# Performance work log

Hardware: AMD Instinct MI355X
Metric: run time of the kernel (lower is better)

The kernel has to match this reference:

```python
import jax, jax.numpy as jnp
import numpy as np

N_NODES = 100000
N_EDGES = 1600000
F_IN, F_HID, F_OUT = 256, 128, 32


def setup_inputs() -> dict:
    key = jax.random.key(0)
    k1, k2, k3, k4 = jax.random.split(key, 4)
    x = jax.random.normal(k1, (N_NODES, F_IN), dtype=jnp.float32)
    edge_index = jax.random.randint(k2, (2, N_EDGES), 0, N_NODES, dtype=jnp.int64)
    W1 = jax.random.normal(k3, (F_IN, F_HID), dtype=jnp.float32) * (1.0 / np.sqrt(F_IN))
    b1 = jnp.zeros((F_HID,), dtype=jnp.float32)
    W2 = jax.random.normal(k4, (F_HID, F_OUT), dtype=jnp.float32) * (1.0 / np.sqrt(F_HID))
    b2 = jnp.zeros((F_OUT,), dtype=jnp.float32)
    return {"x": x, "edge_index": edge_index, "W1": W1, "b1": b1, "W2": W2, "b2": b2}


def _gcn_norm(edge_index, num_nodes):
    # Add self-loops, then symmetric normalization deg^-1/2[src] * deg^-1/2[dst].
    loops = jnp.arange(num_nodes, dtype=edge_index.dtype)
    src = jnp.concatenate([edge_index[0], loops])
    dst = jnp.concatenate([edge_index[1], loops])
    deg = jax.ops.segment_sum(jnp.ones_like(dst, dtype=jnp.float32), dst,
                              num_segments=num_nodes)
    dinv = jnp.where(deg > 0, jax.lax.rsqrt(deg), 0.0)
    norm = dinv[src] * dinv[dst]  # [E + N]
    return src, dst, norm


def _gcn_conv(h, src, dst, norm, num_nodes):
    # h already linearly transformed. Gather sources, scale, scatter-add to dst.
    msgs = h[src] * norm[:, None]
    return jax.ops.segment_sum(msgs, dst, num_segments=num_nodes)


def reference(x, edge_index, W1, b1, W2, b2):
    n = x.shape[0]
    src, dst, norm = _gcn_norm(edge_index, n)
    # Layer 1: linear -> normalized scatter-add -> bias -> relu
    h = _gcn_conv(x @ W1, src, dst, norm, n) + b1
    h = jax.nn.relu(h)
    # F.dropout with training=False (eval mode) is identity.
    # Layer 2
    out = _gcn_conv(h @ W2, src, dst, norm, n) + b2
    return jax.nn.log_softmax(out, axis=1)
```

## Files before the change

kernel.cpp:

```cpp
#include <hip/hip_runtime.h>

#define N_NODES 100000
#define N_EDGES 1600000
#define F_IN 256
#define F_HID 128
#define F_OUT 32
#define NBUCK 391
#define BIN_BLOCKS 512
#define EDGES_PER_BIN 3125

typedef unsigned short ushort_t;
typedef unsigned int uint_t;

using short8  = __attribute__((ext_vector_type(8))) short;
using floatx4 = __attribute__((ext_vector_type(4))) float;

__device__ __forceinline__ ushort_t f2bf(float f) {
    uint_t u = __float_as_uint(f);
    u += 0x7fff + ((u >> 16) & 1);
    return (ushort_t)(u >> 16);
}
__device__ __forceinline__ float bf_lo(uint_t u) { return __uint_as_float(u << 16); }
__device__ __forceinline__ float bf_hi(uint_t u) { return __uint_as_float(u & 0xffff0000u); }
__device__ __forceinline__ uint_t bfpack_trunc(float a, float b) {
    return __builtin_amdgcn_perm(__float_as_uint(b), __float_as_uint(a), 0x07060302u);
}

__global__ __launch_bounds__(256) void histwt_kernel(const int* __restrict__ ei,
                                                     int* __restrict__ bucket_cnt,
                                                     const float* __restrict__ W1,
                                                     const float* __restrict__ W2,
                                                     ushort_t* __restrict__ W1T,
                                                     ushort_t* __restrict__ W2T) {
    __shared__ int h[NBUCK];
    if (blockIdx.x < BIN_BLOCKS) {
        for (int i = threadIdx.x; i < NBUCK; i += 256) h[i] = 0;
        __syncthreads();
        int gid = blockIdx.x * 256 + threadIdx.x;
        for (int e = gid; e < N_EDGES; e += BIN_BLOCKS * 256)
            atomicAdd(&h[ei[N_EDGES + e] >> 8], 1);
        __syncthreads();
        for (int i = threadIdx.x; i < NBUCK; i += 256) {
            int c = h[i];
            if (c) atomicAdd(&bucket_cnt[i], c);
        }
    } else {
        int t = (blockIdx.x - BIN_BLOCKS) * 256 + threadIdx.x;
#pragma unroll
        for (int j = 0; j < 4; j++) {
            int e = j * 8192 + t;
            int n = e >> 8, k = e & 255;
            W1T[e] = f2bf(W1[k * F_HID + n]);
        }
        if (t < 4096) {
            int n = t >> 7, k = t & 127;
            W2T[t] = f2bf(W2[k * F_OUT + n]);
        }
    }
}

__global__ __launch_bounds__(512) void scan_kernel(const int* __restrict__ bucket_cnt,
                                                   int* __restrict__ bucket_base,
                                                   int* __restrict__ bucket_cursor,
                                                   int* __restrict__ offs) {
    __shared__ int s[512];
    int t = threadIdx.x;
    int own = (t < NBUCK) ? bucket_cnt[t] : 0;
    s[t] = own;
    __syncthreads();
    for (int off = 1; off < 512; off <<= 1) {
        int v = (t >= off) ? s[t - off] : 0;
        __syncthreads();
        s[t] += v;
        __syncthreads();
    }
    if (t < NBUCK) {
        int ex = s[t] - own;
        bucket_base[t] = ex;
        bucket_cursor[t] = ex;
    }
    if (t == 0) {
        bucket_base[NBUCK] = N_EDGES;
        offs[N_NODES] = N_EDGES;
    }
}

__global__ __launch_bounds__(256) void bin_kernel(const int* __restrict__ ei,
                                                  int* __restrict__ bucket_cursor,
                                                  int2* __restrict__ binned) {
    __shared__ int h[NBUCK];
    __shared__ int base[NBUCK];
    const int t = threadIdx.x;
    const int beg = blockIdx.x * EDGES_PER_BIN;
    const int end = beg + EDGES_PER_BIN;
    for (int i = t; i < NBUCK; i += 256) h[i] = 0;
    __syncthreads();
    for (int e = beg + t; e < end; e += 256) atomicAdd(&h[ei[N_EDGES + e] >> 8], 1);
    __syncthreads();
    for (int i = t; i < NBUCK; i += 256) {
        int c = h[i];
        base[i] = c ? atomicAdd(&bucket_cursor[i], c) : 0;
        h[i] = 0;
    }
    __syncthreads();
    for (int e = beg + t; e < end; e += 256) {
        int s = ei[e], d = ei[N_EDGES + e];
        int bk = d >> 8;
        int p = base[bk] + atomicAdd(&h[bk], 1);
        binned[p] = make_int2(s, d);
    }
}

__global__ __launch_bounds__(256) void build_kernel(const int2* __restrict__ binned,
                                                    const int* __restrict__ bucket_base,
                                                    int* __restrict__ offs,
                                                    int* __restrict__ csr,
                                                    float* __restrict__ dinv,
                                                    int* __restrict__ degarr) {
    __shared__ int h[256];
    __shared__ int sc[256];
    __shared__ int cur[256];
    const int b = blockIdx.x, t = threadIdx.x;
    const int beg = bucket_base[b];
    const int end = bucket_base[b + 1];
    h[t] = 0;
    __syncthreads();
    for (int j = beg + t; j < end; j += 256) {
        int2 p = binned[j];
        atomicAdd(&h[p.y & 255], 1);
    }
    __syncthreads();
    int deg = h[t];
    sc[t] = deg;
    __syncthreads();
    for (int off = 1; off < 256; off <<= 1) {
        int v = (t >= off) ? sc[t - off] : 0;
        __syncthreads();
        sc[t] += v;
        __syncthreads();
    }
    int excl = sc[t] - deg;
    cur[t] = excl;
    int node = b * 256 + t;
    if (node < N_NODES) {
        offs[node] = beg + excl;
        dinv[node] = rsqrtf((float)deg + 1.0f);
        degarr[node] = deg;
    }
    __syncthreads();
    for (int j = beg + t; j < end; j += 256) {
        int2 p = binned[j];
        int pos = atomicAdd(&cur[p.y & 255], 1);
        csr[beg + pos] = p.x;
    }
}

__global__ __launch_bounds__(256) void pack_kernel(int* __restrict__ csr,
                                                   const int* __restrict__ degarr) {
    int i = blockIdx.x * 256 + threadIdx.x;
    if (i >= N_EDGES / 4) return;
    int4 c = ((int4*)csr)[i];
    c.x |= degarr[c.x] << 20;
    c.y |= degarr[c.y] << 20;
    c.z |= degarr[c.z] << 20;
    c.w |= degarr[c.w] << 20;
    ((int4*)csr)[i] = c;
}

__global__ __launch_bounds__(512) void gemm1_kernel(const float* __restrict__ x,
                                                    const ushort_t* __restrict__ W1T,
                                                    ushort_t* __restrict__ h0a,
                                                    ushort_t* __restrict__ h0b) {
    __shared__ ushort_t Bst[F_HID][F_IN + 8];
    const int tid = threadIdx.x;
    const int rbase = blockIdx.x * 128;
    const int w = tid >> 6;
    const int lane = tid & 63;
    const int q = lane >> 4;
    const int nloc = lane & 15;

#pragma unroll
    for (int j = 0; j < 8; j++) {
        int f = j * 512 + tid;
        int n = f >> 5, kg = f & 31;
        uint4 v = ((const uint4*)(W1T + n * F_IN))[kg];
        *(uint4*)(&Bst[n][kg * 8]) = v;
    }
    __syncthreads();

    const int rowA = rbase + w * 16 + nloc;
    const bool okA = rowA < N_NODES;
    const float* ap = x + (size_t)rowA * F_IN + q * 8;

    floatx4 acc[8];
#pragma unroll
    for (int t = 0; t < 8; t++) acc[t] = (floatx4){0.f, 0.f, 0.f, 0.f};

#pragma unroll
    for (int k0 = 0; k0 < F_IN; k0 += 32) {
        float4 f0 = make_float4(0.f, 0.f, 0.f, 0.f);
        float4 f1 = make_float4(0.f, 0.f, 0.f, 0.f);
        if (okA) {
            f0 = *(const float4*)(ap + k0);
            f1 = *(const float4*)(ap + k0 + 4);
        }
        uint4 au;
        au.x = bfpack_trunc(f0.x, f0.y);
        au.y = bfpack_trunc(f0.z, f0.w);
        au.z = bfpack_trunc(f1.x, f1.y);
        au.w = bfpack_trunc(f1.z, f1.w);
        short8 a = *(short8*)&au;
#pragma unroll
        for (int t = 0; t < 8; t++) {
            short8 b = *(const short8*)(&Bst[t * 16 + nloc][k0 + q * 8]);
            acc[t] = __builtin_amdgcn_mfma_f32_16x16x32_bf16(a, b, acc[t], 0, 0, 0);
        }
    }

#pragma unroll
    for (int reg = 0; reg < 4; reg++) {
        int rowD = rbase + w * 16 + q * 4 + reg;
        if (rowD < N_NODES) {
            ushort_t* opA = h0a + (size_t)rowD * 64 + nloc;
            ushort_t* opB = h0b + (size_t)rowD * 64 + nloc;
#pragma unroll
            for (int t = 0; t < 4; t++) opA[t * 16] = f2bf(acc[t][reg]);
#pragma unroll
            for (int t = 4; t < 8; t++) opB[(t - 4) * 16] = f2bf(acc[t][reg]);
        }
    }
}

__global__ __launch_bounds__(256) void gather64(const ushort_t* __restrict__ tab,
                                                const int* __restrict__ offs,
                                                const int* __restrict__ csr,
                                                const float* __restrict__ dinv,
                                                ushort_t* __restrict__ outt) {
    const int node = blockIdx.x * 8 + (threadIdx.x >> 5);
    const int l = threadIdx.x & 31;
    const int sub = l >> 3;
    const int fl = l & 7;
    const float dn = dinv[node];
    const uint4* rowbase = (const uint4*)tab;

    uint4 sv = rowbase[(size_t)node * 8 + fl];
    float s = (sub == 0) ? dn * dn : 0.f;
    float a[8];
    a[0] = bf_lo(sv.x) * s; a[1] = bf_hi(sv.x) * s;
    a[2] = bf_lo(sv.y) * s; a[3] = bf_hi(sv.y) * s;
    a[4] = bf_lo(sv.z) * s; a[5] = bf_hi(sv.z) * s;
    a[6] = bf_lo(sv.w) * s; a[7] = bf_hi(sv.w) * s;

    const int beg = offs[node], end = offs[node + 1];
    for (int j = beg; j < end; j += 16) {
        uint_t w[4];
        float nn[4];
        uint4 r[4];
#pragma unroll
        for (int k = 0; k < 4; k++) w[k] = ((const uint_t*)csr)[j + 4 * k + sub];
#pragma unroll
        for (int k = 0; k < 4; k++) {
            bool v = (j + 4 * k + sub) < end;
            int src = v ? (int)(w[k] & 0xFFFFFu) : 0;
            nn[k] = v ? rsqrtf((float)(w[k] >> 20) + 1.0f) * dn : 0.f;
            r[k] = rowbase[(size_t)src * 8 + fl];
        }
#pragma unroll
        for (int k = 0; k < 4; k++) {
            float n = nn[k];
            a[0] += bf_lo(r[k].x) * n; a[1] += bf_hi(r[k].x) * n;
            a[2] += bf_lo(r[k].y) * n; a[3] += bf_hi(r[k].y) * n;
            a[4] += bf_lo(r[k].z) * n; a[5] += bf_hi(r[k].z) * n;
            a[6] += bf_lo(r[k].w) * n; a[7] += bf_hi(r[k].w) * n;
        }
    }
#pragma unroll
    for (int i = 0; i < 8; i++) {
        a[i] += __shfl_xor(a[i], 8);
        a[i] += __shfl_xor(a[i], 16);
    }
    if (sub == 0) {
        uint4 p;
        p.x = (uint_t)f2bf(a[0]) | ((uint_t)f2bf(a[1]) << 16);
        p.y = (uint_t)f2bf(a[2]) | ((uint_t)f2bf(a[3]) << 16);
        p.z = (uint_t)f2bf(a[4]) | ((uint_t)f2bf(a[5]) << 16);
        p.w = (uint_t)f2bf(a[6]) | ((uint_t)f2bf(a[7]) << 16);
        ((uint4*)outt)[(size_t)node * 8 + fl] = p;
    }
}

__global__ __launch_bounds__(256) void gemm2_kernel(const ushort_t* __restrict__ aggA,
                                                    const ushort_t* __restrict__ aggB,
                                                    const float* __restrict__ b1,
                                                    const ushort_t* __restrict__ W2T,
                                                    ushort_t* __restrict__ h2bf) {
    __shared__ ushort_t Bs[F_OUT][F_HID + 8];
    __shared__ float b1s[F_HID];
    const int tid = threadIdx.x;
    const int rbase = blockIdx.x * 64;
    const int w = tid >> 6;
    const int lane = tid & 63;
    const int q = lane >> 4;
    const int nloc = lane & 15;

    if (tid < F_HID) b1s[tid] = b1[tid];
#pragma unroll
    for (int jj = 0; jj < 2; jj++) {
        int f = jj * 256 + tid;
        int n = f >> 4, kg = f & 15;
        uint4 v = ((const uint4*)(W2T + n * F_HID))[kg];
        *(uint4*)(&Bs[n][kg * 8]) = v;
    }
    __syncthreads();

    const int rowA = rbase + w * 16 + nloc;
    const bool okA = rowA < N_NODES;

    floatx4 acc[2];
    acc[0] = (floatx4){0.f, 0.f, 0.f, 0.f};
    acc[1] = (floatx4){0.f, 0.f, 0.f, 0.f};

#pragma unroll
    for (int k0 = 0; k0 < F_HID; k0 += 32) {
        int kk = k0 + q * 8;
        const ushort_t* at = (k0 < 64) ? aggA : aggB;
        int kloc = (k0 < 64) ? kk : kk - 64;
        uint4 av = make_uint4(0, 0, 0, 0);
        if (okA) av = *(const uint4*)(at + (size_t)rowA * 64 + kloc);
        float4 bb0 = *(const float4*)(&b1s[kk]);
        float4 bb1 = *(const float4*)(&b1s[kk + 4]);
        uint4 au;
        au.x = bfpack_trunc(fmaxf(bf_lo(av.x) + bb0.x, 0.f), fmaxf(bf_hi(av.x) + bb0.y, 0.f));
        au.y = bfpack_trunc(fmaxf(bf_lo(av.y) + bb0.z, 0.f), fmaxf(bf_hi(av.y) + bb0.w, 0.f));
        au.z = bfpack_trunc(fmaxf(bf_lo(av.z) + bb1.x, 0.f), fmaxf(bf_hi(av.z) + bb1.y, 0.f));
        au.w = bfpack_trunc(fmaxf(bf_lo(av.w) + bb1.z, 0.f), fmaxf(bf_hi(av.w) + bb1.w, 0.f));
        short8 a = *(short8*)&au;
#pragma unroll
        for (int t = 0; t < 2; t++) {
            short8 b = *(const short8*)(&Bs[t * 16 + nloc][kk]);
            acc[t] = __builtin_amdgcn_mfma_f32_16x16x32_bf16(a, b, acc[t], 0, 0, 0);
        }
    }
#pragma unroll
    for (int reg = 0; reg < 4; reg++) {
        int rowD = rbase + w * 16 + q * 4 + reg;
        if (rowD < N_NODES) {
            ushort_t* op = h2bf + (size_t)rowD * F_OUT + nloc;
            op[0]  = f2bf(acc[0][reg]);
            op[16] = f2bf(acc[1][reg]);
        }
    }
}

__global__ __launch_bounds__(256) void gather32_lsm(const ushort_t* __restrict__ h2bf,
                                                    const int* __restrict__ offs,
                                                    const int* __restrict__ csr,
                                                    const float* __restrict__ dinv,
                                                    const float* __restrict__ b2,
                                                    float* __restrict__ out) {
    const int node = blockIdx.x * 8 + (threadIdx.x >> 5);
    const int l = threadIdx.x & 31;
    const int sub = l >> 2;
    const int fl = l & 3;
    const float dn = dinv[node];
    const uint4* rowbase = (const uint4*)h2bf;

    uint4 sv = rowbase[(size_t)node * 4 + fl];
    float s = (sub == 0) ? dn * dn : 0.f;
    float a[8];
    a[0] = bf_lo(sv.x) * s; a[1] = bf_hi(sv.x) * s;
    a[2] = bf_lo(sv.y) * s; a[3] = bf_hi(sv.y) * s;
    a[4] = bf_lo(sv.z) * s; a[5] = bf_hi(sv.z) * s;
    a[6] = bf_lo(sv.w) * s; a[7] = bf_hi(sv.w) * s;

    const int beg = offs[node], end = offs[node + 1];
    for (int j = beg; j < end; j += 16) {
        uint_t w[2];
        float nn[2];
        uint4 r[2];
#pragma unroll
        for (int k = 0; k < 2; k++) w[k] = ((const uint_t*)csr)[j + 8 * k + sub];
#pragma unroll
        for (int k = 0; k < 2; k++) {
            bool v = (j + 8 * k + sub) < end;
            int src = v ? (int)(w[k] & 0xFFFFFu) : 0;
            nn[k] = v ? rsqrtf((float)(w[k] >> 20) + 1.0f) * dn : 0.f;
            r[k] = rowbase[(size_t)src * 4 + fl];
        }
#pragma unroll
        for (int k = 0; k < 2; k++) {
            float n = nn[k];
            a[0] += bf_lo(r[k].x) * n; a[1] += bf_hi(r[k].x) * n;
            a[2] += bf_lo(r[k].y) * n; a[3] += bf_hi(r[k].y) * n;
            a[4] += bf_lo(r[k].z) * n; a[5] += bf_hi(r[k].z) * n;
            a[6] += bf_lo(r[k].w) * n; a[7] += bf_hi(r[k].w) * n;
        }
    }
#pragma unroll
    for (int i = 0; i < 8; i++) {
        a[i] += __shfl_xor(a[i], 4);
        a[i] += __shfl_xor(a[i], 8);
        a[i] += __shfl_xor(a[i], 16);
    }
    float4 bb0 = ((const float4*)b2)[fl * 2];
    float4 bb1 = ((const float4*)b2)[fl * 2 + 1];
    a[0] += bb0.x; a[1] += bb0.y; a[2] += bb0.z; a[3] += bb0.w;
    a[4] += bb1.x; a[5] += bb1.y; a[6] += bb1.z; a[7] += bb1.w;

    float m = a[0];
#pragma unroll
    for (int i = 1; i < 8; i++) m = fmaxf(m, a[i]);
    m = fmaxf(m, __shfl_xor(m, 1));
    m = fmaxf(m, __shfl_xor(m, 2));
    float es = 0.f;
#pragma unroll
    for (int i = 0; i < 8; i++) es += __expf(a[i] - m);
    es += __shfl_xor(es, 1);
    es += __shfl_xor(es, 2);
    float lse = m + __logf(es);

    if (sub == 0) {
        float4 o0 = make_float4(a[0] - lse, a[1] - lse, a[2] - lse, a[3] - lse);
        float4 o1 = make_float4(a[4] - lse, a[5] - lse, a[6] - lse, a[7] - lse);
        float4* op = (float4*)(out + (size_t)node * F_OUT);
        op[fl * 2] = o0;
        op[fl * 2 + 1] = o1;
    }
}

extern "C" void kernel_launch(void* const* d_in, const int* in_sizes, int n_in,
                              void* d_out, int out_size, void* d_ws, size_t ws_size,
                              hipStream_t stream) {
    const float* x  = (const float*)d_in[0];
    const int*   ei = (const int*)d_in[1];
    const float* W1 = (const float*)d_in[2];
    const float* b1 = (const float*)d_in[3];
    const float* W2 = (const float*)d_in[4];
    const float* b2 = (const float*)d_in[5];
    float* out = (float*)d_out;

    float* ws = (float*)d_ws;
    float*    dinv          = ws;
    int*      offs          = (int*)(ws + 100096);
    int*      bucket_cnt    = (int*)(ws + 200224);
    int*      bucket_base   = (int*)(ws + 200736);
    int*      bucket_cursor = (int*)(ws + 201248);
    int*      degarr        = (int*)(ws + 201760);
    int*      csr           = (int*)(ws + 301856);
    ushort_t* W1T           = (ushort_t*)(ws + 1901856);
    ushort_t* W2T           = (ushort_t*)(ws + 1918240);
    ushort_t* h0a           = (ushort_t*)(ws + 1920288);
    ushort_t* h0b           = (ushort_t*)(ws + 5120288);
    ushort_t* aggA          = (ushort_t*)(ws + 8320288);
    ushort_t* aggB          = (ushort_t*)(ws + 11520288);
    ushort_t* h2bf          = (ushort_t*)(ws + 14720288);
    int2*     binned        = (int2*)aggA;

    hipMemsetAsync(bucket_cnt, 0, 512 * sizeof(int), stream);
    histwt_kernel<<<BIN_BLOCKS + 32, 256, 0, stream>>>(ei, bucket_cnt, W1, W2, W1T, W2T);
    scan_kernel<<<1, 512, 0, stream>>>(bucket_cnt, bucket_base, bucket_cursor, offs);
    bin_kernel<<<BIN_BLOCKS, 256, 0, stream>>>(ei, bucket_cursor, binned);
    build_kernel<<<NBUCK, 256, 0, stream>>>(binned, bucket_base, offs, csr, dinv, degarr);
    pack_kernel<<<(N_EDGES / 4 + 255) / 256, 256, 0, stream>>>(csr, degarr);
    gemm1_kernel<<<(N_NODES + 127) / 128, 512, 0, stream>>>(x, W1T, h0a, h0b);
    gather64<<<N_NODES / 8, 256, 0, stream>>>(h0a, offs, csr, dinv, aggA);
    gather64<<<N_NODES / 8, 256, 0, stream>>>(h0b, offs, csr, dinv, aggB);
    gemm2_kernel<<<(N_NODES + 63) / 64, 256, 0, stream>>>(aggA, aggB, b1, W2T, h2bf);
    gather32_lsm<<<N_NODES / 8, 256, 0, stream>>>(h2bf, offs, csr, dinv, b2, out);
}
```

Baseline: 350.9 us.

## Co-launch edge binning with GEMM1 and merge two gather launches into one

The edge-binning work and the first dense GEMM now share a single launch: low block indices do binning and the rest compute 64-row GEMM tiles with 256 threads, so the independent memory-bound and MFMA-bound stages can overlap. The two per-half gather64 launches are merged into one grid of twice the size that picks its input and output table by block index. This removes launch gaps and tail effects. In exchange, GEMM blocks are smaller, each block reloads W1T into LDS, and the binning blocks reserve the large LDS allocation, which can lower their occupancy.

```diff
diff --git a/kernel.cpp b/kernel.cpp
--- a/kernel.cpp
+++ b/kernel.cpp
@@ -8,6 +8,7 @@
 #define NBUCK 391
 #define BIN_BLOCKS 512
 #define EDGES_PER_BIN 3125
+#define G1_BLOCKS 1563
 
 typedef unsigned short ushort_t;
 typedef unsigned int uint_t;
@@ -85,29 +86,94 @@
     }
 }
 
-__global__ __launch_bounds__(256) void bin_kernel(const int* __restrict__ ei,
-                                                  int* __restrict__ bucket_cursor,
-                                                  int2* __restrict__ binned) {
-    __shared__ int h[NBUCK];
-    __shared__ int base[NBUCK];
-    const int t = threadIdx.x;
-    const int beg = blockIdx.x * EDGES_PER_BIN;
-    const int end = beg + EDGES_PER_BIN;
-    for (int i = t; i < NBUCK; i += 256) h[i] = 0;
-    __syncthreads();
-    for (int e = beg + t; e < end; e += 256) atomicAdd(&h[ei[N_EDGES + e] >> 8], 1);
-    __syncthreads();
-    for (int i = t; i < NBUCK; i += 256) {
-        int c = h[i];
-        base[i] = c ? atomicAdd(&bucket_cursor[i], c) : 0;
-        h[i] = 0;
-    }
-    __syncthreads();
-    for (int e = beg + t; e < end; e += 256) {
-        int s = ei[e], d = ei[N_EDGES + e];
-        int bk = d >> 8;
-        int p = base[bk] + atomicAdd(&h[bk], 1);
-        binned[p] = make_int2(s, d);
+__global__ __launch_bounds__(256) void bin_gemm1_kernel(const int* __restrict__ ei,
+                                                        int* __restrict__ bucket_cursor,
+                                                        int2* __restrict__ binned,
+                                                        const float* __restrict__ x,
+                                                        const ushort_t* __restrict__ W1T,
+                                                        ushort_t* __restrict__ h0a,
+                                                        ushort_t* __restrict__ h0b) {
+    __shared__ __align__(16) char smem[(size_t)F_HID * (F_IN + 8) * 2];
+    const int tid = threadIdx.x;
+    if (blockIdx.x < BIN_BLOCKS) {
+        int* h    = (int*)smem;
+        int* base = ((int*)smem) + NBUCK;
+        const int beg = blockIdx.x * EDGES_PER_BIN;
+        const int end = beg + EDGES_PER_BIN;
+        for (int i = tid; i < NBUCK; i += 256) h[i] = 0;
+        __syncthreads();
+        for (int e = beg + tid; e < end; e += 256) atomicAdd(&h[ei[N_EDGES + e] >> 8], 1);
+        __syncthreads();
+        for (int i = tid; i < NBUCK; i += 256) {
+            int c = h[i];
+            base[i] = c ? atomicAdd(&bucket_cursor[i], c) : 0;
+            h[i] = 0;
+        }
+        __syncthreads();
+        for (int e = beg + tid; e < end; e += 256) {
+            int s = ei[e], d = ei[N_EDGES + e];
+            int bk = d >> 8;
+            int p = base[bk] + atomicAdd(&h[bk], 1);
+            binned[p] = make_int2(s, d);
+        }
+    } else {
+        ushort_t (*Bst)[F_IN + 8] = (ushort_t(*)[F_IN + 8])smem;
+        const int rbase = (blockIdx.x - BIN_BLOCKS) * 64;
+        const int w = tid >> 6;
+        const int lane = tid & 63;
+        const int q = lane >> 4;
+        const int nloc = lane & 15;
+
+#pragma unroll
+        for (int j = 0; j < 16; j++) {
+            int f = j * 256 + tid;
+            int n = f >> 5, kg = f & 31;
+            uint4 v = ((const uint4*)(W1T + n * F_IN))[kg];
+            *(uint4*)(&Bst[n][kg * 8]) = v;
+        }
+        __syncthreads();
+
+        const int rowA = rbase + w * 16 + nloc;
+        const bool okA = rowA < N_NODES;
+        const float* ap = x + (size_t)rowA * F_IN + q * 8;
+
+        floatx4 acc[8];
+#pragma unroll
+        for (int t = 0; t < 8; t++) acc[t] = (floatx4){0.f, 0.f, 0.f, 0.f};
+
+#pragma unroll
+        for (int k0 = 0; k0 < F_IN; k0 += 32) {
+            float4 f0 = make_float4(0.f, 0.f, 0.f, 0.f);
+            float4 f1 = make_float4(0.f, 0.f, 0.f, 0.f);
+            if (okA) {
+                f0 = *(const float4*)(ap + k0);
+                f1 = *(const float4*)(ap + k0 + 4);
+            }
+            uint4 au;
+            au.x = bfpack_trunc(f0.x, f0.y);
+            au.y = bfpack_trunc(f0.z, f0.w);
+            au.z = bfpack_trunc(f1.x, f1.y);
+            au.w = bfpack_trunc(f1.z, f1.w);
+            short8 a = *(short8*)&au;
+#pragma unroll
+            for (int t = 0; t < 8; t++) {
+                short8 b = *(const short8*)(&Bst[t * 16 + nloc][k0 + q * 8]);
+                acc[t] = __builtin_amdgcn_mfma_f32_16x16x32_bf16(a, b, acc[t], 0, 0, 0);
+            }
+        }
+
+#pragma unroll
+        for (int reg = 0; reg < 4; reg++) {
+            int rowD = rbase + w * 16 + q * 4 + reg;
+            if (rowD < N_NODES) {
+                ushort_t* opA = h0a + (size_t)rowD * 64 + nloc;
+                ushort_t* opB = h0b + (size_t)rowD * 64 + nloc;
+#pragma unroll
+                for (int t = 0; t < 4; t++) opA[t * 16] = f2bf(acc[t][reg]);
+#pragma unroll
+                for (int t = 4; t < 8; t++) opB[(t - 4) * 16] = f2bf(acc[t][reg]);
+            }
+        }
     }
 }
 
@@ -167,76 +233,19 @@
     ((int4*)csr)[i] = c;
 }
 
-__global__ __launch_bounds__(512) void gemm1_kernel(const float* __restrict__ x,
-                                                    const ushort_t* __restrict__ W1T,
-                                                    ushort_t* __restrict__ h0a,
-                                                    ushort_t* __restrict__ h0b) {
-    __shared__ ushort_t Bst[F_HID][F_IN + 8];
-    const int tid = threadIdx.x;
-    const int rbase = blockIdx.x * 128;
-    const int w = tid >> 6;
-    const int lane = tid & 63;
-    const int q = lane >> 4;
-    const int nloc = lane & 15;
-
-#pragma unroll
-    for (int j = 0; j < 8; j++) {
-        int f = j * 512 + tid;
-        int n = f >> 5, kg = f & 31;
-        uint4 v = ((const uint4*)(W1T + n * F_IN))[kg];
-        *(uint4*)(&Bst[n][kg * 8]) = v;
-    }
-    __syncthreads();
-
-    const int rowA = rbase + w * 16 + nloc;
-    const bool okA = rowA < N_NODES;
-    const float* ap = x + (size_t)rowA * F_IN + q * 8;
-
-    floatx4 acc[8];
-#pragma unroll
-    for (int t = 0; t < 8; t++) acc[t] = (floatx4){0.f, 0.f, 0.f, 0.f};
-
-#pragma unroll
-    for (int k0 = 0; k0 < F_IN; k0 += 32) {
-        float4 f0 = make_float4(0.f, 0.f, 0.f, 0.f);
-        float4 f1 = make_float4(0.f, 0.f, 0.f, 0.f);
-        if (okA) {
-            f0 = *(const float4*)(ap + k0);
-            f1 = *(const float4*)(ap + k0 + 4);
-        }
-        uint4 au;
-        au.x = bfpack_trunc(f0.x, f0.y);
-        au.y = bfpack_trunc(f0.z, f0.w);
-        au.z = bfpack_trunc(f1.x, f1.y);
-        au.w = bfpack_trunc(f1.z, f1.w);
-        short8 a = *(short8*)&au;
-#pragma unroll
-        for (int t = 0; t < 8; t++) {
-            short8 b = *(const short8*)(&Bst[t * 16 + nloc][k0 + q * 8]);
-            acc[t] = __builtin_amdgcn_mfma_f32_16x16x32_bf16(a, b, acc[t], 0, 0, 0);
-        }
-    }
-
-#pragma unroll
-    for (int reg = 0; reg < 4; reg++) {
-        int rowD = rbase + w * 16 + q * 4 + reg;
-        if (rowD < N_NODES) {
-            ushort_t* opA = h0a + (size_t)rowD * 64 + nloc;
-            ushort_t* opB = h0b + (size_t)rowD * 64 + nloc;
-#pragma unroll
-            for (int t = 0; t < 4; t++) opA[t * 16] = f2bf(acc[t][reg]);
-#pragma unroll
-            for (int t = 4; t < 8; t++) opB[(t - 4) * 16] = f2bf(acc[t][reg]);
-        }
-    }
-}
-
-__global__ __launch_bounds__(256) void gather64(const ushort_t* __restrict__ tab,
+__global__ __launch_bounds__(256) void gather64(const ushort_t* __restrict__ h0a,
+                                                const ushort_t* __restrict__ h0b,
                                                 const int* __restrict__ offs,
                                                 const int* __restrict__ csr,
                                                 const float* __restrict__ dinv,
-                                                ushort_t* __restrict__ outt) {
-    const int node = blockIdx.x * 8 + (threadIdx.x >> 5);
+                                                ushort_t* __restrict__ aggA,
+                                                ushort_t* __restrict__ aggB) {
+    const int half = blockIdx.x >= (N_NODES / 8);
+    const int nb = blockIdx.x - half * (N_NODES / 8);
+    const ushort_t* tab = half ? h0b : h0a;
+    ushort_t* outt = half ? aggB : aggA;
+
+    const int node = nb * 8 + (threadIdx.x >> 5);
     const int l = threadIdx.x & 31;
     const int sub = l >> 3;
     const int fl = l & 7;
@@ -459,12 +468,11 @@
     hipMemsetAsync(bucket_cnt, 0, 512 * sizeof(int), stream);
     histwt_kernel<<<BIN_BLOCKS + 32, 256, 0, stream>>>(ei, bucket_cnt, W1, W2, W1T, W2T);
     scan_kernel<<<1, 512, 0, stream>>>(bucket_cnt, bucket_base, bucket_cursor, offs);
-    bin_kernel<<<BIN_BLOCKS, 256, 0, stream>>>(ei, bucket_cursor, binned);
+    bin_gemm1_kernel<<<BIN_BLOCKS + G1_BLOCKS, 256, 0, stream>>>(ei, bucket_cursor, binned,
+                                                                 x, W1T, h0a, h0b);
     build_kernel<<<NBUCK, 256, 0, stream>>>(binned, bucket_base, offs, csr, dinv, degarr);
     pack_kernel<<<(N_EDGES / 4 + 255) / 256, 256, 0, stream>>>(csr, degarr);
-    gemm1_kernel<<<(N_NODES + 127) / 128, 512, 0, stream>>>(x, W1T, h0a, h0b);
-    gather64<<<N_NODES / 8, 256, 0, stream>>>(h0a, offs, csr, dinv, aggA);
-    gather64<<<N_NODES / 8, 256, 0, stream>>>(h0b, offs, csr, dinv, aggB);
+    gather64<<<2 * (N_NODES / 8), 256, 0, stream>>>(h0a, h0b, offs, csr, dinv, aggA, aggB);
     gemm2_kernel<<<(N_NODES + 63) / 64, 256, 0, stream>>>(aggA, aggB, b1, W2T, h2bf);
     gather32_lsm<<<N_NODES / 8, 256, 0, stream>>>(h2bf, offs, csr, dinv, b2, out);
 }
```

Measured after the change: 339.9 us. 3.1% less time.
